# Optimization experiments

Hardware: AMD Instinct MI355X
Metric: run time of the kernel (lower is better)

Reference implementation:

```python
import jax, jax.numpy as jnp
import numpy as np


def setup_inputs() -> dict:
    key = jax.random.key(0)
    k1, k2, k3 = jax.random.split(key, 3)
    B, C, H, W = 512, 4, 125, 125
    img = jax.random.normal(k1, (B, C, H, W), dtype=jnp.float32)
    # fc: Linear(62500 -> 20), Tanh, Dropout(eval=identity), Linear(20 -> 1), Sigmoid
    W1 = jax.random.normal(k2, (C * H * W, 20), dtype=jnp.float32) * 0.004  # ~1/sqrt(62500)
    b1 = jnp.zeros((20,), dtype=jnp.float32)
    W2 = jax.random.normal(k3, (20, 1), dtype=jnp.float32) * 0.2
    b2 = jnpp = jnp.zeros((1,), dtype=jnp.float32)
    return {"img": img, "W1": W1, "b1": b1, "W2": W2, "b2": b2}


def reference(img, W1, b1, W2, b2):
    B, C, H, W = img.shape
    # small MLP -> rotation angle theta in [0, 2*pi)
    h = jnp.tanh(img.reshape(B, -1) @ W1 + b1)          # (B, 20)
    theta = jax.nn.sigmoid(h @ W2 + b2)[:, 0] * (2.0 * np.pi)  # (B,)
    c, s = jnp.cos(theta), jnp.sin(theta)
    z = jnp.zeros_like(c)
    # (B, 2, 3) affine matrix: pure rotation, zero translation
    Mat = jnp.stack([jnp.stack([c, -s, z], axis=-1),
                     jnp.stack([s,  c, z], axis=-1)], axis=-2)

    # affine_grid, align_corners=True: normalized coords span [-1, 1] at pixel centers
    ys = jnp.linspace(-1.0, 1.0, H, dtype=img.dtype)
    xs = jnp.linspace(-1.0, 1.0, W, dtype=img.dtype)
    gy, gx = jnp.meshgrid(ys, xs, indexing="ij")        # (H, W)
    base = jnp.stack([gx, gy, jnp.ones_like(gx)], axis=-1)  # (H, W, 3) homogeneous (x, y, 1)
    grid = jnp.einsum("bij,hwj->bhwi", Mat, base)       # (B, H, W, 2) -> (x, y)

    # grid_sample: bilinear, padding_mode='zeros', align_corners=True
    ix = (grid[..., 0] + 1.0) * 0.5 * (W - 1)
    iy = (grid[..., 1] + 1.0) * 0.5 * (H - 1)
    ix0 = jnp.floor(ix); iy0 = jnp.floor(iy)
    ix1 = ix0 + 1.0;     iy1 = iy0 + 1.0
    wx1 = ix - ix0; wx0 = 1.0 - wx1
    wy1 = iy - iy0; wy0 = 1.0 - wy1

    def gather(ixi, iyi):
        valid = (ixi >= 0) & (ixi <= W - 1) & (iyi >= 0) & (iyi <= H - 1)
        xc = jnp.clip(ixi, 0, W - 1).astype(jnp.int32)
        yc = jnp.clip(iyi, 0, H - 1).astype(jnp.int32)
        vals = jax.vmap(lambda im, yy, xx: im[:, yy, xx])(img, yc, xc)  # (B, C, H, W)
        return vals * valid[:, None, :, :].astype(img.dtype)

    out = (gather(ix0, iy0) * (wx0 * wy0)[:, None]
         + gather(ix1, iy0) * (wx1 * wy0)[:, None]
         + gather(ix0, iy1) * (wx0 * wy1)[:, None]
         + gather(ix1, iy1) * (wx1 * wy1)[:, None])
    return out, Mat
```

## Files before the change

kernel.cpp:

```cpp
#include <hip/hip_runtime.h>
#include <hip/hip_bf16.h>
#include <math.h>

#define K_TOT 62500
#define KQ_TOT 15625
#define NJ    20
#define NB    512
#define HW_   15625
#define WW_   125
#define NKSPL 128
#define LDSTR 68

#define HP_OFF   0
#define HRED_OFF (NKSPL * NJ * NB)
#define W1T_OFF  2000000
#define MAT_OFF  32000000

__global__ __launch_bounds__(256) void k0_transpose(const float* __restrict__ W1,
                                                    float* __restrict__ W1T) {
    const int k = blockIdx.x * 256 + threadIdx.x;
    if (k >= K_TOT) return;
    const float* src = W1 + (size_t)k * NJ;
#pragma unroll
    for (int j = 0; j < NJ; ++j)
        W1T[(size_t)j * K_TOT + k] = src[j];
}

__global__ __launch_bounds__(256, 4) void k1_partial(const float* __restrict__ img,
                                                     const float* __restrict__ W1T,
                                                     float* __restrict__ hpart) {
    __shared__ float simg[2][64 * LDSTR];
    const int tid  = threadIdx.x;
    const int bx   = blockIdx.x;
    const int b0   = blockIdx.y << 6;
    const int lane = tid & 63;
    const int j0   = __builtin_amdgcn_readfirstlane((tid >> 6) * 5);
    const int srow = tid >> 4;
    const int squad = tid & 15;

    const int q0  = (int)(((long long)bx * KQ_TOT) >> 7);
    const int q1  = (int)(((long long)(bx + 1) * KQ_TOT) >> 7);
    const int nqb = q1 - q0;
    const int nsteps = (nqb + 15) >> 4;

    const float4* img4 = reinterpret_cast<const float4*>(img);
    const float4* W1T4 = reinterpret_cast<const float4*>(W1T);
    const float4* wj0 = W1T4 + (size_t)(j0 + 0) * KQ_TOT;
    const float4* wj1 = W1T4 + (size_t)(j0 + 1) * KQ_TOT;
    const float4* wj2 = W1T4 + (size_t)(j0 + 2) * KQ_TOT;
    const float4* wj3 = W1T4 + (size_t)(j0 + 3) * KQ_TOT;
    const float4* wj4 = W1T4 + (size_t)(j0 + 4) * KQ_TOT;

    float acc0 = 0.f, acc1 = 0.f, acc2 = 0.f, acc3 = 0.f, acc4 = 0.f;

    {
        const int qg = q0 + squad;
#pragma unroll
        for (int rr = 0; rr < 4; ++rr) {
            const int row = srow + (rr << 4);
            *reinterpret_cast<float4*>(&simg[0][row * LDSTR + (squad << 2)]) =
                img4[(size_t)(b0 + row) * KQ_TOT + qg];
        }
    }
    __syncthreads();

    int cur = 0;
    for (int s = 0; s < nsteps; ++s) {
        float4 r0, r1, r2, r3;
        bool dl = false;
        if (s + 1 < nsteps) {
            const int rem = nqb - (s + 1) * 16;
            const int cq  = (rem < 16) ? rem : 16;
            if (squad < cq) {
                dl = true;
                const size_t qg = (size_t)q0 + (s + 1) * 16 + squad;
                r0 = img4[(size_t)(b0 + srow +  0) * KQ_TOT + qg];
                r1 = img4[(size_t)(b0 + srow + 16) * KQ_TOT + qg];
                r2 = img4[(size_t)(b0 + srow + 32) * KQ_TOT + qg];
                r3 = img4[(size_t)(b0 + srow + 48) * KQ_TOT + qg];
            }
        }

        {
            const int rem = nqb - s * 16;
            const float* simgl = &simg[cur][lane * LDSTR];
            const int qb = q0 + s * 16;
            if (rem >= 16) {
#pragma unroll
                for (int q = 0; q < 16; ++q) {
                    const float4 iv = *reinterpret_cast<const float4*>(&simgl[q << 2]);
                    const int qi = qb + q;
                    const float4 w0 = wj0[qi];
                    const float4 w1 = wj1[qi];
                    const float4 w2 = wj2[qi];
                    const float4 w3 = wj3[qi];
                    const float4 w4 = wj4[qi];
                    acc0 += iv.x * w0.x + iv.y * w0.y + iv.z * w0.z + iv.w * w0.w;
                    acc1 += iv.x * w1.x + iv.y * w1.y + iv.z * w1.z + iv.w * w1.w;
                    acc2 += iv.x * w2.x + iv.y * w2.y + iv.z * w2.z + iv.w * w2.w;
                    acc3 += iv.x * w3.x + iv.y * w3.y + iv.z * w3.z + iv.w * w3.w;
                    acc4 += iv.x * w4.x + iv.y * w4.y + iv.z * w4.z + iv.w * w4.w;
                }
            } else {
                for (int q = 0; q < rem; ++q) {
                    const float4 iv = *reinterpret_cast<const float4*>(&simgl[q << 2]);
                    const int qi = qb + q;
                    const float4 w0 = wj0[qi];
                    const float4 w1 = wj1[qi];
                    const float4 w2 = wj2[qi];
                    const float4 w3 = wj3[qi];
                    const float4 w4 = wj4[qi];
                    acc0 += iv.x * w0.x + iv.y * w0.y + iv.z * w0.z + iv.w * w0.w;
                    acc1 += iv.x * w1.x + iv.y * w1.y + iv.z * w1.z + iv.w * w1.w;
                    acc2 += iv.x * w2.x + iv.y * w2.y + iv.z * w2.z + iv.w * w2.w;
                    acc3 += iv.x * w3.x + iv.y * w3.y + iv.z * w3.z + iv.w * w3.w;
                    acc4 += iv.x * w4.x + iv.y * w4.y + iv.z * w4.z + iv.w * w4.w;
                }
            }
        }

        if (dl) {
            float* d = &simg[cur ^ 1][srow * LDSTR + (squad << 2)];
            *reinterpret_cast<float4*>(&d[ 0 * LDSTR]) = r0;
            *reinterpret_cast<float4*>(&d[16 * LDSTR]) = r1;
            *reinterpret_cast<float4*>(&d[32 * LDSTR]) = r2;
            *reinterpret_cast<float4*>(&d[48 * LDSTR]) = r3;
        }
        __syncthreads();
        cur ^= 1;
    }

    const int b = b0 + lane;
    float* dst = &hpart[(size_t)(bx * NJ + j0) * NB + b];
    dst[0 * NB] = acc0;
    dst[1 * NB] = acc1;
    dst[2 * NB] = acc2;
    dst[3 * NB] = acc3;
    dst[4 * NB] = acc4;
}

__global__ __launch_bounds__(256) void k2_reduce(const float* __restrict__ hpart,
                                                 float* __restrict__ hred) {
    const int b = blockIdx.x * 256 + threadIdx.x;
    const int j = blockIdx.y;
    float a = 0.f;
#pragma unroll 8
    for (int c = 0; c < NKSPL; ++c)
        a += hpart[(size_t)(c * NJ + j) * NB + b];
    hred[j * NB + b] = a;
}

__global__ __launch_bounds__(256) void k2_head(const float* __restrict__ hred,
                                               const float* __restrict__ b1,
                                               const float* __restrict__ W2,
                                               const float* __restrict__ b2,
                                               float* __restrict__ mat) {
    const int b = blockIdx.x * 256 + threadIdx.x;
    float z = b2[0];
#pragma unroll
    for (int j = 0; j < NJ; ++j) {
        const float h = tanhf(hred[j * NB + b] + b1[j]);
        z += h * W2[j];
    }
    const float sg = 1.0f / (1.0f + expf(-z));
    const float theta = sg * 6.28318530717958647692f;
    float sn, cn;
    sincosf(theta, &sn, &cn);
    float* m = mat + (size_t)b * 6;
    m[0] = cn; m[1] = -sn; m[2] = 0.f;
    m[3] = sn; m[4] = cn;  m[5] = 0.f;
}

__device__ __forceinline__ unsigned int pack2bf(float a, float b) {
    __hip_bfloat16 ha = __float2bfloat16(a);
    __hip_bfloat16 hb = __float2bfloat16(b);
    const unsigned int ua = (unsigned int)__builtin_bit_cast(unsigned short, ha);
    const unsigned int ub = (unsigned int)__builtin_bit_cast(unsigned short, hb);
    return ua | (ub << 16);
}
#define BF_LO(u) __uint_as_float((u) << 16)
#define BF_HI(u) __uint_as_float((u) & 0xffff0000u)

template <bool FUSED>
__global__ __launch_bounds__(1024) void k3_sample_t(const float* __restrict__ img,
                                                    const float* __restrict__ hpart_or_mat,
                                                    const float* __restrict__ b1,
                                                    const float* __restrict__ W2,
                                                    const float* __restrict__ b2,
                                                    float* __restrict__ out) {
    __shared__ uint2 sch[HW_];
    __shared__ float sred[NJ + 2];
    const int b   = blockIdx.x;
    const int tid = threadIdx.x;

    float cb, sb;
    if (FUSED) {
        if (tid < 640) {
            const int j = tid >> 5;
            const int l = tid & 31;
            float part = 0.f;
#pragma unroll
            for (int i = 0; i < 4; ++i) {
                const int c = (l << 2) + i;
                part += hpart_or_mat[(size_t)(c * NJ + j) * NB + b];
            }
#pragma unroll
            for (int m = 16; m; m >>= 1)
                part += __shfl_xor(part, m);
            if (l == 0) sred[j] = part;
        }
        __syncthreads();
        if (tid == 0) {
            float z = b2[0];
#pragma unroll
            for (int j = 0; j < NJ; ++j)
                z += tanhf(sred[j] + b1[j]) * W2[j];
            const float sg = 1.0f / (1.0f + expf(-z));
            float sn, cn;
            sincosf(sg * 6.28318530717958647692f, &sn, &cn);
            float* m = out + MAT_OFF + (size_t)b * 6;
            m[0] = cn; m[1] = -sn; m[2] = 0.f;
            m[3] = sn; m[4] = cn;  m[5] = 0.f;
            sred[NJ]     = cn;
            sred[NJ + 1] = sn;
        }
        __syncthreads();
        cb = sred[NJ];
        sb = sred[NJ + 1];
    } else {
        cb = hpart_or_mat[(size_t)b * 6 + 4];
        sb = hpart_or_mat[(size_t)b * 6 + 3];
    }

    const size_t ib = (size_t)b * 4 * HW_;
    const float* p0 = img + ib;
    const float* p1 = p0 + HW_;
    const float* p2 = p1 + HW_;
    const float* p3 = p2 + HW_;

    for (int i = tid; i < HW_; i += 1024) {
        uint2 q;
        q.x = pack2bf(p0[i], p1[i]);
        q.y = pack2bf(p2[i], p3[i]);
        sch[i] = q;
    }
    __syncthreads();

    float* o0 = out + ib;
    for (int p = tid; p < HW_; p += 1024) {
        const int y = p / WW_;
        const int x = p - y * WW_;

        const float gx = (float)x * (1.0f / 62.0f) - 1.0f;
        const float gy = (float)y * (1.0f / 62.0f) - 1.0f;
        const float fx = (cb * gx - sb * gy + 1.0f) * 62.0f;
        const float fy = (sb * gx + cb * gy + 1.0f) * 62.0f;

        const float x0f = floorf(fx), y0f = floorf(fy);
        const int x0 = (int)x0f, y0 = (int)y0f;
        const int x1 = x0 + 1, y1 = y0 + 1;
        const float wx1 = fx - x0f, wx0 = 1.0f - wx1;
        const float wy1 = fy - y0f, wy0 = 1.0f - wy1;

        const bool vx0 = ((unsigned)x0 <= 124u);
        const bool vx1 = ((unsigned)x1 <= 124u);
        const bool vy0 = ((unsigned)y0 <= 124u);
        const bool vy1 = ((unsigned)y1 <= 124u);

        const int cx0 = min(max(x0, 0), 124), cx1 = min(max(x1, 0), 124);
        const int cy0 = min(max(y0, 0), 124), cy1 = min(max(y1, 0), 124);

        const float m00 = (vx0 && vy0) ? wx0 * wy0 : 0.f;
        const float m01 = (vx1 && vy0) ? wx1 * wy0 : 0.f;
        const float m10 = (vx0 && vy1) ? wx0 * wy1 : 0.f;
        const float m11 = (vx1 && vy1) ? wx1 * wy1 : 0.f;

        const uint2 q00 = sch[cy0 * WW_ + cx0];
        const uint2 q01 = sch[cy0 * WW_ + cx1];
        const uint2 q10 = sch[cy1 * WW_ + cx0];
        const uint2 q11 = sch[cy1 * WW_ + cx1];

        float a0, a1, a2, a3;
        a0  = BF_LO(q00.x) * m00;  a1  = BF_HI(q00.x) * m00;
        a2  = BF_LO(q00.y) * m00;  a3  = BF_HI(q00.y) * m00;
        a0 += BF_LO(q01.x) * m01;  a1 += BF_HI(q01.x) * m01;
        a2 += BF_LO(q01.y) * m01;  a3 += BF_HI(q01.y) * m01;
        a0 += BF_LO(q10.x) * m10;  a1 += BF_HI(q10.x) * m10;
        a2 += BF_LO(q10.y) * m10;  a3 += BF_HI(q10.y) * m10;
        a0 += BF_LO(q11.x) * m11;  a1 += BF_HI(q11.x) * m11;
        a2 += BF_LO(q11.y) * m11;  a3 += BF_HI(q11.y) * m11;

        o0[p]            = a0;
        o0[p + 1 * HW_]  = a1;
        o0[p + 2 * HW_]  = a2;
        o0[p + 3 * HW_]  = a3;
    }
}

extern "C" void kernel_launch(void* const* d_in, const int* in_sizes, int n_in,
                              void* d_out, int out_size, void* d_ws, size_t ws_size,
                              hipStream_t stream) {
    const float* img = (const float*)d_in[0];
    const float* W1  = (const float*)d_in[1];
    const float* b1  = (const float*)d_in[2];
    const float* W2  = (const float*)d_in[3];
    const float* b2  = (const float*)d_in[4];
    float* out = (float*)d_out;

    float* W1T = out + W1T_OFF;
    const size_t hp_bytes = (size_t)NKSPL * NJ * NB * sizeof(float);

    hipLaunchKernelGGL(k0_transpose, dim3((K_TOT + 255) / 256), dim3(256), 0, stream, W1, W1T);

    if (ws_size >= hp_bytes) {
        float* hpart = (float*)d_ws;
        hipLaunchKernelGGL(k1_partial, dim3(NKSPL, 8), dim3(256), 0, stream, img, W1T, hpart);
        hipLaunchKernelGGL(k3_sample_t<true>, dim3(NB), dim3(1024), 0, stream,
                           img, hpart, b1, W2, b2, out);
    } else {
        float* hpart = out + HP_OFF;
        float* hred  = out + HRED_OFF;
        float* mat   = out + MAT_OFF;
        hipLaunchKernelGGL(k1_partial, dim3(NKSPL, 8), dim3(256), 0, stream, img, W1T, hpart);
        hipLaunchKernelGGL(k2_reduce, dim3(2, NJ), dim3(256), 0, stream, hpart, hred);
        hipLaunchKernelGGL(k2_head, dim3(2), dim3(256), 0, stream, hred, b1, W2, b2, mat);
        hipLaunchKernelGGL(k3_sample_t<false>, dim3(NB), dim3(1024), 0, stream,
                           img, mat, b1, W2, b2, out);
    }
}
```

Measured before the change: 106.5 us.

## Deepen k1 image prefetch to two stages and vectorize bf16 staging loads

The partial-GEMV kernel's 8-step loop is now fully unrolled with two register buffers, so image tiles are fetched two steps ahead instead of one. This hides more global-load latency behind the FMA work, at the cost of extra registers. The rotation kernel now stages the image into shared memory with float4 loads per channel plus a scalar tail element, which cuts the number of load instructions. Channel planes 1 to 3 sit 4 bytes past a 16-byte boundary, so those float4 loads are misaligned; this relies on unaligned global access being supported and may be slower than aligned loads.

```diff
diff --git a/kernel.cpp b/kernel.cpp
--- a/kernel.cpp
+++ b/kernel.cpp
@@ -25,6 +25,28 @@
     for (int j = 0; j < NJ; ++j)
         W1T[(size_t)j * K_TOT + k] = src[j];
 }
+
+#define K1_ISSUE(t, R, DL)                                                   \
+    {                                                                        \
+        const int cq_ = ((t) == 7) ? (nqb - 112) : 16;                       \
+        DL = (squad < cq_);                                                  \
+        if (DL) {                                                            \
+            const size_t qg_ = (size_t)q0 + (t) * 16 + squad;                \
+            R[0] = img4[(size_t)(b0 + srow +  0) * KQ_TOT + qg_];            \
+            R[1] = img4[(size_t)(b0 + srow + 16) * KQ_TOT + qg_];            \
+            R[2] = img4[(size_t)(b0 + srow + 32) * KQ_TOT + qg_];            \
+            R[3] = img4[(size_t)(b0 + srow + 48) * KQ_TOT + qg_];            \
+        }                                                                    \
+    }
+
+#define K1_WRITE(t, R, DL)                                                   \
+    if (DL) {                                                                \
+        float* d_ = &simg[(t) & 1][srow * LDSTR + (squad << 2)];             \
+        *reinterpret_cast<float4*>(&d_[ 0 * LDSTR]) = R[0];                  \
+        *reinterpret_cast<float4*>(&d_[16 * LDSTR]) = R[1];                  \
+        *reinterpret_cast<float4*>(&d_[32 * LDSTR]) = R[2];                  \
+        *reinterpret_cast<float4*>(&d_[48 * LDSTR]) = R[3];                  \
+    }
 
 __global__ __launch_bounds__(256, 4) void k1_partial(const float* __restrict__ img,
                                                      const float* __restrict__ W1T,
@@ -41,7 +63,6 @@
     const int q0  = (int)(((long long)bx * KQ_TOT) >> 7);
     const int q1  = (int)(((long long)(bx + 1) * KQ_TOT) >> 7);
     const int nqb = q1 - q0;
-    const int nsteps = (nqb + 15) >> 4;
 
     const float4* img4 = reinterpret_cast<const float4*>(img);
     const float4* W1T4 = reinterpret_cast<const float4*>(W1T);
@@ -53,39 +74,28 @@
 
     float acc0 = 0.f, acc1 = 0.f, acc2 = 0.f, acc3 = 0.f, acc4 = 0.f;
 
-    {
-        const int qg = q0 + squad;
-#pragma unroll
-        for (int rr = 0; rr < 4; ++rr) {
-            const int row = srow + (rr << 4);
-            *reinterpret_cast<float4*>(&simg[0][row * LDSTR + (squad << 2)]) =
-                img4[(size_t)(b0 + row) * KQ_TOT + qg];
-        }
-    }
+    float4 RA[4], RB[4];
+    bool dlA = false, dlB = false;
+
+    K1_ISSUE(0, RA, dlA);
+    K1_ISSUE(1, RB, dlB);
+    K1_WRITE(0, RA, dlA);
     __syncthreads();
 
-    int cur = 0;
-    for (int s = 0; s < nsteps; ++s) {
-        float4 r0, r1, r2, r3;
-        bool dl = false;
-        if (s + 1 < nsteps) {
-            const int rem = nqb - (s + 1) * 16;
-            const int cq  = (rem < 16) ? rem : 16;
-            if (squad < cq) {
-                dl = true;
-                const size_t qg = (size_t)q0 + (s + 1) * 16 + squad;
-                r0 = img4[(size_t)(b0 + srow +  0) * KQ_TOT + qg];
-                r1 = img4[(size_t)(b0 + srow + 16) * KQ_TOT + qg];
-                r2 = img4[(size_t)(b0 + srow + 32) * KQ_TOT + qg];
-                r3 = img4[(size_t)(b0 + srow + 48) * KQ_TOT + qg];
-            }
+#pragma unroll
+    for (int s = 0; s < 8; ++s) {
+        if ((s & 1) == 0) {
+            if (s + 2 < 8) K1_ISSUE(s + 2, RA, dlA);
+            if (s + 1 < 8) K1_WRITE(s + 1, RB, dlB);
+        } else {
+            if (s + 2 < 8) K1_ISSUE(s + 2, RB, dlB);
+            if (s + 1 < 8) K1_WRITE(s + 1, RA, dlA);
         }
 
         {
-            const int rem = nqb - s * 16;
-            const float* simgl = &simg[cur][lane * LDSTR];
+            const float* simgl = &simg[s & 1][lane * LDSTR];
             const int qb = q0 + s * 16;
-            if (rem >= 16) {
+            if (s < 7) {
 #pragma unroll
                 for (int q = 0; q < 16; ++q) {
                     const float4 iv = *reinterpret_cast<const float4*>(&simgl[q << 2]);
@@ -102,6 +112,7 @@
                     acc4 += iv.x * w4.x + iv.y * w4.y + iv.z * w4.z + iv.w * w4.w;
                 }
             } else {
+                const int rem = nqb - 112;
                 for (int q = 0; q < rem; ++q) {
                     const float4 iv = *reinterpret_cast<const float4*>(&simgl[q << 2]);
                     const int qi = qb + q;
@@ -118,16 +129,7 @@
                 }
             }
         }
-
-        if (dl) {
-            float* d = &simg[cur ^ 1][srow * LDSTR + (squad << 2)];
-            *reinterpret_cast<float4*>(&d[ 0 * LDSTR]) = r0;
-            *reinterpret_cast<float4*>(&d[16 * LDSTR]) = r1;
-            *reinterpret_cast<float4*>(&d[32 * LDSTR]) = r2;
-            *reinterpret_cast<float4*>(&d[48 * LDSTR]) = r3;
-        }
         __syncthreads();
-        cur ^= 1;
     }
 
     const int b = b0 + lane;
@@ -238,11 +240,27 @@
     const float* p2 = p1 + HW_;
     const float* p3 = p2 + HW_;
 
-    for (int i = tid; i < HW_; i += 1024) {
-        uint2 q;
-        q.x = pack2bf(p0[i], p1[i]);
-        q.y = pack2bf(p2[i], p3[i]);
-        sch[i] = q;
+    {
+        const float4* v0 = reinterpret_cast<const float4*>(p0);
+        const float4* v1 = reinterpret_cast<const float4*>(p1);
+        const float4* v2 = reinterpret_cast<const float4*>(p2);
+        const float4* v3 = reinterpret_cast<const float4*>(p3);
+        const int nv = HW_ >> 2;
+        for (int i = tid; i < nv; i += 1024) {
+            const float4 a = v0[i];
+            const float4 bq = v1[i];
+            const float4 c = v2[i];
+            const float4 d = v3[i];
+            const int base = i << 2;
+            sch[base + 0] = make_uint2(pack2bf(a.x, bq.x), pack2bf(c.x, d.x));
+            sch[base + 1] = make_uint2(pack2bf(a.y, bq.y), pack2bf(c.y, d.y));
+            sch[base + 2] = make_uint2(pack2bf(a.z, bq.z), pack2bf(c.z, d.z));
+            sch[base + 3] = make_uint2(pack2bf(a.w, bq.w), pack2bf(c.w, d.w));
+        }
+        if (tid == 0) {
+            sch[HW_ - 1] = make_uint2(pack2bf(p0[HW_ - 1], p1[HW_ - 1]),
+                                      pack2bf(p2[HW_ - 1], p3[HW_ - 1]));
+        }
     }
     __syncthreads();
 
```

New measurement: 328.5 us. 3.08x slower.
